# Optimization experiments

Measured on AMD Instinct MI355X. Metric: run time of the kernel, lower is better.

## Reference

```python
import jax, jax.numpy as jnp
import numpy as np

N, NODE_DIM, EDGE_DIM, HID, NREL = 1024, 128, 32, 128, 16


def _sage(h, adj, W, b):
    # agg = mean over (weighted) neighbors: (adj @ h) / (deg + 1e-6)
    agg = (adj @ h) / (jnp.sum(adj, axis=1, keepdims=True) + 1e-6)
    return jax.nn.relu(jnp.concatenate([h, agg], axis=1) @ W.T + b)


def setup_inputs() -> dict:
    key = jax.random.key(0)
    ks = jax.random.split(key, 12)
    s1 = 1.0 / np.sqrt(2 * NODE_DIM)
    s2 = 1.0 / np.sqrt(2 * HID)
    s3 = 1.0 / np.sqrt(2 * HID + EDGE_DIM)
    s4 = 1.0 / np.sqrt(HID)
    return {
        "node_feat": jax.random.normal(ks[0], (N, NODE_DIM), jnp.float32),
        "edge_feat": jax.random.normal(ks[1], (N, N, EDGE_DIM), jnp.float32),
        "adj": jax.random.uniform(ks[2], (N, N), jnp.float32),
        "W_g1": jax.random.normal(ks[3], (HID, 2 * NODE_DIM), jnp.float32) * s1,
        "b_g1": jax.random.normal(ks[4], (HID,), jnp.float32) * s1,
        "W_g2": jax.random.normal(ks[5], (HID, 2 * HID), jnp.float32) * s2,
        "b_g2": jax.random.normal(ks[6], (HID,), jnp.float32) * s2,
        "W_c1": jax.random.normal(ks[7], (HID, 2 * HID + EDGE_DIM), jnp.float32) * s3,
        "b_c1": jax.random.normal(ks[8], (HID,), jnp.float32) * s3,
        "W_c2": jax.random.normal(ks[9], (NREL, HID), jnp.float32) * s4,
        "b_c2": jax.random.normal(ks[10], (NREL,), jnp.float32) * s4,
    }


def reference(node_feat, edge_feat, adj, W_g1, b_g1, W_g2, b_g2, W_c1, b_c1, W_c2, b_c2):
    h = _sage(node_feat, adj, W_g1, b_g1)          # [N, HID]
    h = _sage(h, adj, W_g2, b_g2)                  # [N, HID]
    H = h.shape[1]
    # Split first classifier layer over [h_i ; h_j ; e_ij] to avoid a huge concat.
    Wa, Wb, We = W_c1[:, :H], W_c1[:, H:2 * H], W_c1[:, 2 * H:]
    pre = ((h @ Wa.T)[:, None, :]
           + (h @ Wb.T)[None, :, :]
           + jnp.einsum('ije,he->ijh', edge_feat, We)
           + b_c1)                                  # [N, N, HID]
    logits = jax.nn.relu(pre) @ W_c2.T + b_c2       # [N, N, NREL]
    # diagonal (i == j) stays zero, matching the skipped loop iterations
    n = logits.shape[0]
    mask = 1.0 - jnp.eye(n, dtype=logits.dtype)
    return logits * mask[:, :, None]
```

## Files before the change

kernel.cpp:

```cpp
#include <hip/hip_runtime.h>
#include <hip/hip_bf16.h>
#include <stdint.h>

constexpr int NN = 1024;
constexpr int DD = 128;
constexpr int EDIM = 32;
constexpr int NR = 16;

using short4v = __attribute__((ext_vector_type(4))) short;
using short8v = __attribute__((ext_vector_type(8))) short;
using f32x4   = __attribute__((ext_vector_type(4))) float;

__device__ __forceinline__ short f2bf(float x) {
  __hip_bfloat16 h = __float2bfloat16(x);
  return __builtin_bit_cast(short, h);
}

__device__ __forceinline__ void nt_store4(float* p, const float4& v) {
  f32x4 t;
  t[0] = v.x; t[1] = v.y; t[2] = v.z; t[3] = v.w;
  __builtin_nontemporal_store(t, (f32x4*)p);
}

__global__ __launch_bounds__(256) void k_adjgemm(const float* __restrict__ adj,
                                                 const float* __restrict__ X,
                                                 float* __restrict__ part) {
  __shared__ float sadj[16][136];
  int t = threadIdx.x;
  int ic = blockIdx.x & 63, kc = blockIdx.x >> 6;
  int i0 = ic * 16, k0 = kc * 128;
  {
    int il = t >> 4;
    int kl = (t & 15) * 8;
    const float4* src = (const float4*)(adj + (size_t)(i0 + il) * NN + k0 + kl);
    *(float4*)&sadj[il][kl]     = src[0];
    *(float4*)&sadj[il][kl + 4] = src[1];
  }
  __syncthreads();
  int hq = (t & 31) * 4;
  int ir = t >> 5;
  float4 acc0 = {0,0,0,0}, acc1 = {0,0,0,0};
  const float* Xb = X + (size_t)k0 * DD + hq;
  #pragma unroll 4
  for (int k = 0; k < 128; ++k) {
    float4 xv = *(const float4*)(Xb + (size_t)k * DD);
    float a0 = sadj[ir][k];
    float a1 = sadj[ir + 8][k];
    acc0.x += a0 * xv.x; acc0.y += a0 * xv.y; acc0.z += a0 * xv.z; acc0.w += a0 * xv.w;
    acc1.x += a1 * xv.x; acc1.y += a1 * xv.y; acc1.z += a1 * xv.z; acc1.w += a1 * xv.w;
  }
  *(float4*)(part + ((size_t)kc * NN + (i0 + ir)) * DD + hq)     = acc0;
  *(float4*)(part + ((size_t)kc * NN + (i0 + ir + 8)) * DD + hq) = acc1;
}

__global__ __launch_bounds__(256) void k_dense1(const float* __restrict__ X,
                                                const float* __restrict__ part,
                                                const float* __restrict__ adj,
                                                const float* __restrict__ W,
                                                const float* __restrict__ b,
                                                float* __restrict__ out,
                                                float* __restrict__ rsinv) {
  __shared__ float sagg[2][128];
  __shared__ float red[4];
  int t = threadIdx.x;
  int ig = t >> 7, h = t & 127;
  int i = blockIdx.x * 2 + ig;
  {
    const float4* ar = (const float4*)(adj + (size_t)i * NN);
    float4 v0 = ar[h * 2], v1 = ar[h * 2 + 1];
    float s = v0.x + v0.y + v0.z + v0.w + v1.x + v1.y + v1.z + v1.w;
    #pragma unroll
    for (int off = 32; off > 0; off >>= 1) s += __shfl_down(s, off, 64);
    if ((t & 63) == 0) red[t >> 6] = s;
  }
  __syncthreads();
  float rs = 1.0f / (red[ig * 2] + red[ig * 2 + 1] + 1e-6f);
  if (h == 0) rsinv[i] = rs;
  {
    float ss = 0.f;
    #pragma unroll
    for (int kc = 0; kc < 8; ++kc) ss += part[(size_t)kc * NN * DD + (size_t)i * DD + h];
    sagg[ig][h] = ss * rs;
  }
  __syncthreads();
  const float4* xr = (const float4*)(X + (size_t)i * DD);
  const float4* ar = (const float4*)(&sagg[ig][0]);
  const float4* w1 = (const float4*)(W + (size_t)h * 256);
  const float4* w2 = (const float4*)(W + (size_t)h * 256 + DD);
  float acc = b[h];
  #pragma unroll 8
  for (int k = 0; k < 32; ++k) {
    float4 x = xr[k], w = w1[k];
    acc += x.x * w.x + x.y * w.y + x.z * w.z + x.w * w.w;
  }
  #pragma unroll 8
  for (int k = 0; k < 32; ++k) {
    float4 y = ar[k], w = w2[k];
    acc += y.x * w.x + y.y * w.y + y.z * w.z + y.w * w.w;
  }
  out[(size_t)i * DD + h] = fmaxf(acc, 0.f);
}

__global__ __launch_bounds__(256) void k_dense2ab(const float* __restrict__ X,
                                                  const float* __restrict__ part,
                                                  const float* __restrict__ rsinv,
                                                  const float* __restrict__ W,
                                                  const float* __restrict__ b,
                                                  const float* __restrict__ Wc1,
                                                  const float* __restrict__ bc1,
                                                  float* __restrict__ Aib,
                                                  float* __restrict__ Bmat) {
  __shared__ float sagg[2][128];
  __shared__ float sh2[2][128];
  int t = threadIdx.x;
  int ig = t >> 7, h = t & 127;
  int i = blockIdx.x * 2 + ig;
  {
    float ss = 0.f;
    #pragma unroll
    for (int kc = 0; kc < 8; ++kc) ss += part[(size_t)kc * NN * DD + (size_t)i * DD + h];
    sagg[ig][h] = ss * rsinv[i];
  }
  __syncthreads();
  {
    const float4* xr = (const float4*)(X + (size_t)i * DD);
    const float4* ar = (const float4*)(&sagg[ig][0]);
    const float4* w1 = (const float4*)(W + (size_t)h * 256);
    const float4* w2 = (const float4*)(W + (size_t)h * 256 + DD);
    float acc = b[h];
    #pragma unroll 8
    for (int k = 0; k < 32; ++k) {
      float4 x = xr[k], w = w1[k];
      acc += x.x * w.x + x.y * w.y + x.z * w.z + x.w * w.w;
    }
    #pragma unroll 8
    for (int k = 0; k < 32; ++k) {
      float4 y = ar[k], w = w2[k];
      acc += y.x * w.x + y.y * w.y + y.z * w.z + y.w * w.w;
    }
    sh2[ig][h] = fmaxf(acc, 0.f);
  }
  __syncthreads();
  const float4* xr = (const float4*)(&sh2[ig][0]);
  const float4* wa = (const float4*)(Wc1 + (size_t)h * 288);
  const float4* wb = (const float4*)(Wc1 + (size_t)h * 288 + 128);
  float aa = bc1[h], bb = 0.f;
  #pragma unroll 8
  for (int k = 0; k < 32; ++k) {
    float4 x = xr[k];
    float4 a = wa[k], b2 = wb[k];
    aa += x.x * a.x + x.y * a.y + x.z * a.z + x.w * a.w;
    bb += x.x * b2.x + x.y * b2.y + x.z * b2.z + x.w * b2.w;
  }
  Aib[(size_t)i * DD + h] = aa;
  Bmat[(size_t)i * DD + h] = bb;
}


#define EDGE_BODY(T, S, PF) do {                                              \
    float4 a_ = eA##S, b_ = eB##S;                                            \
    if (PF) {                                                                 \
      const float* p_ = ebl + (size_t)((T) + 6) * ((size_t)NN * EDIM);        \
      eA##S = *(const float4*)p_;                                             \
      eB##S = *(const float4*)(p_ + 4);                                       \
    }                                                                         \
    short8v ef_;                                                              \
    ef_[0]=f2bf(a_.x); ef_[1]=f2bf(a_.y); ef_[2]=f2bf(a_.z); ef_[3]=f2bf(a_.w); \
    ef_[4]=f2bf(b_.x); ef_[5]=f2bf(b_.y); ef_[6]=f2bf(b_.z); ef_[7]=f2bf(b_.w); \
    char* pw_ = psm + (((T) & 1) << 12);                                      \
    const float* ap_ = aibs + (T) * 128 + 4 * g;                              \
    _Pragma("unroll")                                                         \
    for (int n = 0; n < 8; ++n) {                                             \
      float4 av_ = *(const float4*)(ap_ + 16 * n);                            \
      f32x4 ci_;                                                              \
      ci_[0] = av_.x + bjv[n].x; ci_[1] = av_.y + bjv[n].y;                   \
      ci_[2] = av_.z + bjv[n].z; ci_[3] = av_.w + bjv[n].w;                   \
      f32x4 acc_ = __builtin_amdgcn_mfma_f32_16x16x32_bf16(weF[n], ef_, ci_, 0, 0, 0); \
      short4v pk_;                                                            \
      pk_[0] = f2bf(fmaxf(acc_[0], 0.f)); pk_[1] = f2bf(fmaxf(acc_[1], 0.f)); \
      pk_[2] = f2bf(fmaxf(acc_[2], 0.f)); pk_[3] = f2bf(fmaxf(acc_[3], 0.f)); \
      *(short4v*)(pw_ + (((n >> 1) << 10) + ((n & 1) << 9) + wroff)) = pk_;   \
    }                                                                         \
  } while (0)

#define G2(G2T, OREG) do {                                                    \
    f32x4 a2_;                                                                \
    a2_[0] = bc2v.x; a2_[1] = bc2v.y; a2_[2] = bc2v.z; a2_[3] = bc2v.w;       \
    const char* pp_ = psm + (((G2T) & 1) << 12);                              \
    _Pragma("unroll")                                                         \
    for (int kk = 0; kk < 4; ++kk) {                                          \
      short8v pb_ = *(const short8v*)(pp_ + ((kk << 10) + rdP));              \
      a2_ = __builtin_amdgcn_mfma_f32_16x16x32_bf16(wcF[kk], pb_, a2_, 0, 0, 0); \
    }                                                                         \
    bool dg_ = (j == i0 + (G2T));                                             \
    OREG.x = dg_ ? 0.f : a2_[0];                                              \
    OREG.y = dg_ ? 0.f : a2_[1];                                              \
    OREG.z = dg_ ? 0.f : a2_[2];                                              \
    OREG.w = dg_ ? 0.f : a2_[3];                                              \
  } while (0)

#define FLUSH(BASE) do {                                                      \
    nt_store4(out + ((size_t)(i0 + (BASE) + 0) * NN + j) * NR + 4 * g, o0);   \
    nt_store4(out + ((size_t)(i0 + (BASE) + 1) * NN + j) * NR + 4 * g, o1);   \
    nt_store4(out + ((size_t)(i0 + (BASE) + 2) * NN + j) * NR + 4 * g, o2);   \
    nt_store4(out + ((size_t)(i0 + (BASE) + 3) * NN + j) * NR + 4 * g, o3);   \
  } while (0)

__global__ __launch_bounds__(256, 1) void k_edge(const float* __restrict__ edge,
                                                 const float* __restrict__ Wc1,
                                                 const float* __restrict__ Wc2,
                                                 const float* __restrict__ bc2,
                                                 const float* __restrict__ Aib,
                                                 const float* __restrict__ Bmat,
                                                 float* __restrict__ out) {
  __shared__ __align__(16) char psm_all[4][2][4096];
  __shared__ __align__(16) float aibs[16 * 128];
  int tid = threadIdx.x;
  int w = tid >> 6, lane = tid & 63;
  int c = lane & 15, g = lane >> 4;
  int ig = blockIdx.x >> 4, jg = blockIdx.x & 15;
  int i0 = ig * 16;
  int j0w = jg * 64 + w * 16;
  int j = j0w + c;

  {
    int ii = tid >> 4, h8 = (tid & 15) * 8;
    const float4* s = (const float4*)(Aib + (size_t)(i0 + ii) * DD + h8);
    *(float4*)(aibs + ii * 128 + h8)     = s[0];
    *(float4*)(aibs + ii * 128 + h8 + 4) = s[1];
  }

  short8v weF[8];
  #pragma unroll
  for (int n = 0; n < 8; ++n) {
    const float* p = Wc1 + (size_t)(16 * n + c) * 288 + 256 + 8 * g;
    float4 f0 = *(const float4*)p;
    float4 f1 = *(const float4*)(p + 4);
    short8v s;
    s[0]=f2bf(f0.x); s[1]=f2bf(f0.y); s[2]=f2bf(f0.z); s[3]=f2bf(f0.w);
    s[4]=f2bf(f1.x); s[5]=f2bf(f1.y); s[6]=f2bf(f1.z); s[7]=f2bf(f1.w);
    weF[n] = s;
  }
  short8v wcF[4];
  #pragma unroll
  for (int kk = 0; kk < 4; ++kk) {
    const float* p = Wc2 + (size_t)c * DD + 32 * kk + 8 * g;
    float4 f0 = *(const float4*)p;
    float4 f1 = *(const float4*)(p + 4);
    short8v s;
    s[0]=f2bf(f0.x); s[1]=f2bf(f0.y); s[2]=f2bf(f0.z); s[3]=f2bf(f0.w);
    s[4]=f2bf(f1.x); s[5]=f2bf(f1.y); s[6]=f2bf(f1.z); s[7]=f2bf(f1.w);
    wcF[kk] = s;
  }
  float4 bc2v = *(const float4*)(bc2 + 4 * g);
  float4 bjv[8];
  #pragma unroll
  for (int n = 0; n < 8; ++n)
    bjv[n] = *(const float4*)(Bmat + (size_t)j * DD + 16 * n + 4 * g);

  __syncthreads();

  char* psm = &psm_all[w][0][0];
  const float* ebl = edge + ((size_t)i0 * NN + j) * EDIM + 8 * g;
  int wroff = (c << 4) + ((g & 1) << 3) + ((g >> 1) << 8);
  int rdP   = (g << 8) + (c << 4);

  float4 o0, o1, o2, o3;

  float4 eA0, eB0, eA1, eB1, eA2, eB2, eA3, eB3, eA4, eB4, eA5, eB5;
  {
    const size_t STP = (size_t)NN * EDIM;
    eA0 = *(const float4*)(ebl);            eB0 = *(const float4*)(ebl + 4);
    eA1 = *(const float4*)(ebl + STP);      eB1 = *(const float4*)(ebl + STP + 4);
    eA2 = *(const float4*)(ebl + 2 * STP);  eB2 = *(const float4*)(ebl + 2 * STP + 4);
    eA3 = *(const float4*)(ebl + 3 * STP);  eB3 = *(const float4*)(ebl + 3 * STP + 4);
    eA4 = *(const float4*)(ebl + 4 * STP);  eB4 = *(const float4*)(ebl + 4 * STP + 4);
    eA5 = *(const float4*)(ebl + 5 * STP);  eB5 = *(const float4*)(ebl + 5 * STP + 4);
  }

  EDGE_BODY(0, 0, 1);
  EDGE_BODY(1, 1, 1);  G2(0, o0);
  EDGE_BODY(2, 2, 1);  G2(1, o1);
  EDGE_BODY(3, 3, 1);  G2(2, o2);
  EDGE_BODY(4, 4, 1);  G2(3, o3);  FLUSH(0);
  EDGE_BODY(5, 5, 1);  G2(4, o0);
  EDGE_BODY(6, 0, 1);  G2(5, o1);
  EDGE_BODY(7, 1, 1);  G2(6, o2);
  EDGE_BODY(8, 2, 1);  G2(7, o3);  FLUSH(4);
  EDGE_BODY(9, 3, 1);  G2(8, o0);
  EDGE_BODY(10, 4, 0); G2(9, o1);
  EDGE_BODY(11, 5, 0); G2(10, o2);
  EDGE_BODY(12, 0, 0); G2(11, o3); FLUSH(8);
  EDGE_BODY(13, 1, 0); G2(12, o0);
  EDGE_BODY(14, 2, 0); G2(13, o1);
  EDGE_BODY(15, 3, 0); G2(14, o2);
  G2(15, o3); FLUSH(12);
}

extern "C" void kernel_launch(void* const* d_in, const int* in_sizes, int n_in,
                              void* d_out, int out_size, void* d_ws, size_t ws_size,
                              hipStream_t stream) {
  const float* node_feat = (const float*)d_in[0];
  const float* edge_feat = (const float*)d_in[1];
  const float* adj  = (const float*)d_in[2];
  const float* W_g1 = (const float*)d_in[3];
  const float* b_g1 = (const float*)d_in[4];
  const float* W_g2 = (const float*)d_in[5];
  const float* b_g2 = (const float*)d_in[6];
  const float* W_c1 = (const float*)d_in[7];
  const float* b_c1 = (const float*)d_in[8];
  const float* W_c2 = (const float*)d_in[9];
  const float* b_c2 = (const float*)d_in[10];
  float* out = (float*)d_out;

  float* ws    = (float*)d_ws;
  float* rsinv = ws;
  float* part  = ws + 1024;
  float* h1    = part + 8 * NN * DD;
  float* Aib   = h1 + NN * DD;
  float* Bmat  = Aib + NN * DD;

  k_adjgemm<<<512, 256, 0, stream>>>(adj, node_feat, part);
  k_dense1<<<512, 256, 0, stream>>>(node_feat, part, adj, W_g1, b_g1, h1, rsinv);
  k_adjgemm<<<512, 256, 0, stream>>>(adj, h1, part);
  k_dense2ab<<<512, 256, 0, stream>>>(h1, part, rsinv, W_g2, b_g2, W_c1, b_c1, Aib, Bmat);
  k_edge<<<1024, 256, 0, stream>>>(edge_feat, W_c1, W_c2, b_c2, Aib, Bmat, out);
}
```

Before: 128.1 us.

## Use bf16 MFMA for adjacency aggregation GEMMs with transposed bf16 features

Replaces the scalar FP32 adjacency GEMM with an MFMA 16x16x32 bf16 kernel. Node features are first transposed and converted to bf16 by a small new kernel. The K split drops from 8 to 4 partial buffers, so the dense kernels sum fewer partials. This trades the FP32 FMA cost for matrix-core throughput, but adds a transpose launch per layer and rounds adj and features to bf16, which loses precision.

```diff
diff --git a/kernel.cpp b/kernel.cpp
--- a/kernel.cpp
+++ b/kernel.cpp
@@ -22,35 +22,64 @@
   __builtin_nontemporal_store(t, (f32x4*)p);
 }
 
-__global__ __launch_bounds__(256) void k_adjgemm(const float* __restrict__ adj,
-                                                 const float* __restrict__ X,
-                                                 float* __restrict__ part) {
-  __shared__ float sadj[16][136];
+__global__ __launch_bounds__(256) void k_transp(const float* __restrict__ src,
+                                                short* __restrict__ dst) {
+  __shared__ float tile[32][33];
+  int b = blockIdx.x;
+  int r0 = (b & 31) * 32, c0 = (b >> 5) * 32;
   int t = threadIdx.x;
-  int ic = blockIdx.x & 63, kc = blockIdx.x >> 6;
-  int i0 = ic * 16, k0 = kc * 128;
-  {
-    int il = t >> 4;
-    int kl = (t & 15) * 8;
-    const float4* src = (const float4*)(adj + (size_t)(i0 + il) * NN + k0 + kl);
-    *(float4*)&sadj[il][kl]     = src[0];
-    *(float4*)&sadj[il][kl + 4] = src[1];
-  }
-  __syncthreads();
-  int hq = (t & 31) * 4;
-  int ir = t >> 5;
-  float4 acc0 = {0,0,0,0}, acc1 = {0,0,0,0};
-  const float* Xb = X + (size_t)k0 * DD + hq;
-  #pragma unroll 4
-  for (int k = 0; k < 128; ++k) {
-    float4 xv = *(const float4*)(Xb + (size_t)k * DD);
-    float a0 = sadj[ir][k];
-    float a1 = sadj[ir + 8][k];
-    acc0.x += a0 * xv.x; acc0.y += a0 * xv.y; acc0.z += a0 * xv.z; acc0.w += a0 * xv.w;
-    acc1.x += a1 * xv.x; acc1.y += a1 * xv.y; acc1.z += a1 * xv.z; acc1.w += a1 * xv.w;
-  }
-  *(float4*)(part + ((size_t)kc * NN + (i0 + ir)) * DD + hq)     = acc0;
-  *(float4*)(part + ((size_t)kc * NN + (i0 + ir + 8)) * DD + hq) = acc1;
+  {
+    int rr = t >> 3, c4 = (t & 7) * 4;
+    float4 v = *(const float4*)(src + (size_t)(r0 + rr) * DD + c0 + c4);
+    tile[rr][c4]     = v.x;
+    tile[rr][c4 + 1] = v.y;
+    tile[rr][c4 + 2] = v.z;
+    tile[rr][c4 + 3] = v.w;
+  }
+  __syncthreads();
+  {
+    int cc = t >> 3, r4 = (t & 7) * 4;
+    short4v s;
+    s[0] = f2bf(tile[r4 + 0][cc]);
+    s[1] = f2bf(tile[r4 + 1][cc]);
+    s[2] = f2bf(tile[r4 + 2][cc]);
+    s[3] = f2bf(tile[r4 + 3][cc]);
+    *(short4v*)(dst + (size_t)(c0 + cc) * NN + r0 + r4) = s;
+  }
+}
+
+__global__ __launch_bounds__(256) void k_adjmm(const short* __restrict__ XT,
+                                               const float* __restrict__ adj,
+                                               float* __restrict__ part) {
+  int t = threadIdx.x;
+  int w = t >> 6, lane = t & 63;
+  int c = lane & 15, g = lane >> 4;
+  int b = blockIdx.x;
+  int ic = b & 15, hc = (b >> 4) & 3, kc = b >> 6;
+  int i0 = ic * 64 + w * 16, h0 = hc * 32;
+  size_t kb = (size_t)kc * 256 + 8 * g;
+
+  f32x4 acc0 = {0, 0, 0, 0}, acc1 = {0, 0, 0, 0};
+  const short* xa0 = XT + (size_t)(h0 + c) * NN + kb;
+  const short* xa1 = XT + (size_t)(h0 + 16 + c) * NN + kb;
+  const float* ba  = adj + (size_t)(i0 + c) * NN + kb;
+  #pragma unroll
+  for (int ks = 0; ks < 8; ++ks) {
+    short8v a0 = *(const short8v*)(xa0 + ks * 32);
+    short8v a1 = *(const short8v*)(xa1 + ks * 32);
+    float4 b0 = *(const float4*)(ba + ks * 32);
+    float4 b1 = *(const float4*)(ba + ks * 32 + 4);
+    short8v bb;
+    bb[0] = f2bf(b0.x); bb[1] = f2bf(b0.y); bb[2] = f2bf(b0.z); bb[3] = f2bf(b0.w);
+    bb[4] = f2bf(b1.x); bb[5] = f2bf(b1.y); bb[6] = f2bf(b1.z); bb[7] = f2bf(b1.w);
+    acc0 = __builtin_amdgcn_mfma_f32_16x16x32_bf16(a0, bb, acc0, 0, 0, 0);
+    acc1 = __builtin_amdgcn_mfma_f32_16x16x32_bf16(a1, bb, acc1, 0, 0, 0);
+  }
+  float* p0 = part + ((size_t)kc * NN + (i0 + c)) * DD + h0 + 4 * g;
+  float4 o0 = {acc0[0], acc0[1], acc0[2], acc0[3]};
+  float4 o1 = {acc1[0], acc1[1], acc1[2], acc1[3]};
+  *(float4*)(p0)      = o0;
+  *(float4*)(p0 + 16) = o1;
 }
 
 __global__ __launch_bounds__(256) void k_dense1(const float* __restrict__ X,
@@ -79,7 +108,7 @@
   {
     float ss = 0.f;
     #pragma unroll
-    for (int kc = 0; kc < 8; ++kc) ss += part[(size_t)kc * NN * DD + (size_t)i * DD + h];
+    for (int kc = 0; kc < 4; ++kc) ss += part[(size_t)kc * NN * DD + (size_t)i * DD + h];
     sagg[ig][h] = ss * rs;
   }
   __syncthreads();
@@ -118,7 +147,7 @@
   {
     float ss = 0.f;
     #pragma unroll
-    for (int kc = 0; kc < 8; ++kc) ss += part[(size_t)kc * NN * DD + (size_t)i * DD + h];
+    for (int kc = 0; kc < 4; ++kc) ss += part[(size_t)kc * NN * DD + (size_t)i * DD + h];
     sagg[ig][h] = ss * rsinv[i];
   }
   __syncthreads();
@@ -155,7 +184,6 @@
   Aib[(size_t)i * DD + h] = aa;
   Bmat[(size_t)i * DD + h] = bb;
 }
-
 
 #define EDGE_BODY(T, S, PF) do {                                              \
     float4 a_ = eA##S, b_ = eB##S;                                            \
@@ -316,13 +344,17 @@
   float* ws    = (float*)d_ws;
   float* rsinv = ws;
   float* part  = ws + 1024;
-  float* h1    = part + 8 * NN * DD;
+  float* h1    = part + 4 * NN * DD;
   float* Aib   = h1 + NN * DD;
   float* Bmat  = Aib + NN * DD;
-
-  k_adjgemm<<<512, 256, 0, stream>>>(adj, node_feat, part);
+  short* XT1   = (short*)(Bmat + NN * DD);
+  short* XT2   = XT1 + DD * NN;
+
+  k_transp<<<128, 256, 0, stream>>>(node_feat, XT1);
+  k_adjmm<<<256, 256, 0, stream>>>(XT1, adj, part);
   k_dense1<<<512, 256, 0, stream>>>(node_feat, part, adj, W_g1, b_g1, h1, rsinv);
-  k_adjgemm<<<512, 256, 0, stream>>>(adj, h1, part);
+  k_transp<<<128, 256, 0, stream>>>(h1, XT2);
+  k_adjmm<<<256, 256, 0, stream>>>(XT2, adj, part);
   k_dense2ab<<<512, 256, 0, stream>>>(h1, part, rsinv, W_g2, b_g2, W_c1, b_c1, Aib, Bmat);
   k_edge<<<1024, 256, 0, stream>>>(edge_feat, W_c1, W_c2, b_c2, Aib, Bmat, out);
 }
```

Measured after the change: 122.8 us. 4.2% less time.
